# Kernel tuning notes

Hardware: AMD Instinct MI355X
Metric: run time of the kernel (lower is better)

## Reference

```python
import jax, jax.numpy as jnp
import numpy as np

EPS = 1e-8  # torch F.cosine_similarity eps


def setup_inputs() -> dict:
    key = jax.random.key(0)
    k1, k2, k3 = jax.random.split(key, 3)
    bn, cn, dim = 4096, 8192, 1024
    x = jax.random.normal(k1, (bn, dim), dtype=jnp.float32)
    positive = jax.random.normal(k2, (bn, dim), dtype=jnp.float32)
    negative = jax.random.normal(k3, (cn, dim), dtype=jnp.float32)
    return {"x": x, "positive": positive, "negative": negative}


def reference(x, positive, negative):
    bn = x.shape[0]
    nx = jnp.linalg.norm(x, axis=1)          # (bn,)
    npos = jnp.linalg.norm(positive, axis=1)  # (bn,)
    nneg = jnp.linalg.norm(negative, axis=1)  # (cn,)
    # positive cosine similarity, torch-style eps clamp on norm product
    sim = jnp.sum(x * positive, axis=1) / jnp.maximum(nx * npos, EPS)  # (bn,)
    # negative cosine similarities via one matmul instead of (bn,cn,dim) repeats
    neg_sim = (x @ negative.T) / jnp.maximum(nx[:, None] * nneg[None, :], EPS)  # (bn,cn)
    p = jnp.exp(sim) / jnp.sum(jnp.exp(neg_sim), axis=1)  # (bn,)
    loss = -jnp.sum(jnp.log(p)) / bn
    return loss
```

## Files before the change

### kernel.cpp

```cpp
#include <hip/hip_runtime.h>
#include <stdint.h>
#include <stddef.h>

#define DIM 1024
#define EPS 1e-8f

typedef __attribute__((ext_vector_type(4)))  int   i32x4;
typedef __attribute__((ext_vector_type(8)))  int   i32x8;
typedef __attribute__((ext_vector_type(4)))  float f32x4;

#define SCALE8 0x7B7B7B7B

__device__ __forceinline__ void async_copy16(const void* g, void* l) {
    __builtin_amdgcn_global_load_lds(
        (__attribute__((address_space(1))) void*)const_cast<void*>(g),
        (__attribute__((address_space(3))) void*)(l), 16, 0, 0);
}

__global__ __launch_bounds__(256)
void prep_all(const float* __restrict__ x, const float* __restrict__ pos,
              const float* __restrict__ neg,
              unsigned char* __restrict__ Xn, unsigned char* __restrict__ Nn,
              float* __restrict__ simOut, float* __restrict__ rowsum, int bn) {
    const int lane = threadIdx.x & 63;
    const int wave = threadIdx.x >> 6;
    const int grow = blockIdx.x * 4 + wave;
    const bool isX = grow < bn;
    const int row  = isX ? grow : grow - bn;
    const float* src = isX ? x : neg;
    unsigned char* dst = isX ? Xn : Nn;

    const float4* s = (const float4*)(src + (size_t)row * DIM);
    float4 xv[4], pv[4];
    float sxx = 0.f, spp = 0.f, sxp = 0.f;
#pragma unroll
    for (int i = 0; i < 4; i++) {
        xv[i] = s[lane + 64 * i];
        sxx += xv[i].x * xv[i].x + xv[i].y * xv[i].y + xv[i].z * xv[i].z + xv[i].w * xv[i].w;
    }
    if (isX) {
        const float4* p = (const float4*)(pos + (size_t)row * DIM);
#pragma unroll
        for (int i = 0; i < 4; i++) {
            pv[i] = p[lane + 64 * i];
            spp += pv[i].x * pv[i].x + pv[i].y * pv[i].y + pv[i].z * pv[i].z + pv[i].w * pv[i].w;
            sxp += xv[i].x * pv[i].x + xv[i].y * pv[i].y + xv[i].z * pv[i].z + xv[i].w * pv[i].w;
        }
#pragma unroll
        for (int off = 1; off < 64; off <<= 1) {
            sxx += __shfl_xor(sxx, off);
            spp += __shfl_xor(spp, off);
            sxp += __shfl_xor(sxp, off);
        }
    } else {
#pragma unroll
        for (int off = 1; off < 64; off <<= 1) sxx += __shfl_xor(sxx, off);
    }
    const float nx  = sqrtf(sxx);
    const float inv = (nx > 0.f) ? (16.f / nx) : 0.f;
    if (isX && lane == 0) {
        const float np = sqrtf(spp);
        simOut[row] = sxp / fmaxf(nx * np, EPS);
        rowsum[row] = 0.f;
    }
    unsigned int t;
    t = __builtin_amdgcn_cvt_pk_fp8_f32(xv[0].x * inv, xv[0].y * inv, 0, false);
    unsigned int q0 = __builtin_amdgcn_cvt_pk_fp8_f32(xv[0].z * inv, xv[0].w * inv, t, true);
    t = __builtin_amdgcn_cvt_pk_fp8_f32(xv[1].x * inv, xv[1].y * inv, 0, false);
    unsigned int q1 = __builtin_amdgcn_cvt_pk_fp8_f32(xv[1].z * inv, xv[1].w * inv, t, true);
    t = __builtin_amdgcn_cvt_pk_fp8_f32(xv[2].x * inv, xv[2].y * inv, 0, false);
    unsigned int q2 = __builtin_amdgcn_cvt_pk_fp8_f32(xv[2].z * inv, xv[2].w * inv, t, true);
    t = __builtin_amdgcn_cvt_pk_fp8_f32(xv[3].x * inv, xv[3].y * inv, 0, false);
    unsigned int q3 = __builtin_amdgcn_cvt_pk_fp8_f32(xv[3].z * inv, xv[3].w * inv, t, true);

    unsigned int* wr = (unsigned int*)(dst + (size_t)row * DIM);
    wr[lane]       = q0;
    wr[lane + 64]  = q1;
    wr[lane + 128] = q2;
    wr[lane + 192] = q3;
}

__global__ __launch_bounds__(256, 3)
void gemm_exp_rowsum(const unsigned char* __restrict__ Xn,
                     const unsigned char* __restrict__ Nn,
                     float* __restrict__ rowsum) {
    constexpr int KB = DIM;
    constexpr int BK = 128;
    __shared__ __align__(16) unsigned char Bsh[3][128 * BK];

    const int tid  = threadIdx.x;
    const int lane = tid & 63;
    const int wave = tid >> 6;

    const int nwg  = gridDim.x * gridDim.y;
    const int bid  = blockIdx.y * gridDim.x + blockIdx.x;
    const int swz  = (bid & 7) * (nwg >> 3) + (bid >> 3);
    const int rowBase = (swz / gridDim.x) * 128;
    const int colBase = (swz % gridDim.x) * 128;

    const int srow = lane >> 3;
    const int sch  = (lane & 7) ^ srow;
    const unsigned char* gB = Nn + (size_t)(colBase + wave * 32 + srow) * KB + sch * 16;

    const f32x4 fz = {0.f, 0.f, 0.f, 0.f};
    f32x4 acc[4][4];
#pragma unroll
    for (int mi = 0; mi < 4; mi++)
#pragma unroll
        for (int ni = 0; ni < 4; ni++) acc[mi][ni] = fz;

    const int m0   = (wave >> 1) * 64;
    const int n0   = (wave & 1) * 64;
    const int mrow = lane & 15;
    const int q    = lane >> 4;
    const int c0   = ((2 * q) ^ (mrow & 7)) << 4;

    const unsigned char* gAbase =
        Xn + (size_t)(rowBase + m0 + mrow) * KB + 32 * q;

    int boff[4];
#pragma unroll
    for (int i = 0; i < 4; i++) boff[i] = (n0 + 16 * i + mrow) * BK + c0;

#define STAGE(buf, stg)                                                        \
    do {                                                                       \
        const int kq = (stg) * BK;                                             \
        _Pragma("unroll")                                                      \
        for (int i = 0; i < 4; i++)                                            \
            async_copy16(gB + (size_t)(8 * i) * KB + kq,                       \
                         &Bsh[buf][(wave * 32 + 8 * i) * BK]);                 \
    } while (0)

    STAGE(0, 0);
    STAGE(1, 1);
    asm volatile("s_waitcnt vmcnt(4)\n\ts_barrier" ::: "memory");

#pragma unroll
    for (int w = 0; w < 8; w++) {
        const unsigned char* Bb = Bsh[w % 3];
        if (w <= 5) STAGE((w + 2) % 3, w + 2);
        const unsigned char* gAw = gAbase + w * BK;
        i32x8 Af[4], Bf[4];
#pragma unroll
        for (int mi = 0; mi < 4; mi++) {
            i32x4 lo = *(const i32x4*)(gAw + (size_t)(16 * mi) * KB);
            i32x4 hi = *(const i32x4*)(gAw + (size_t)(16 * mi) * KB + 16);
            Af[mi] = __builtin_shufflevector(lo, hi, 0, 1, 2, 3, 4, 5, 6, 7);
        }
#pragma unroll
        for (int i = 0; i < 4; i++) {
            i32x4 lo = *(const i32x4*)(Bb + boff[i]);
            i32x4 hi = *(const i32x4*)(Bb + (boff[i] ^ 16));
            Bf[i] = __builtin_shufflevector(lo, hi, 0, 1, 2, 3, 4, 5, 6, 7);
        }
        __builtin_amdgcn_s_setprio(1);
#pragma unroll
        for (int mi = 0; mi < 4; mi++)
#pragma unroll
            for (int ni = 0; ni < 4; ni++)
                acc[mi][ni] = __builtin_amdgcn_mfma_scale_f32_16x16x128_f8f6f4(
                    Af[mi], Bf[ni], acc[mi][ni], 0, 0, 0, SCALE8, 0, SCALE8);
        __builtin_amdgcn_s_setprio(0);
        if (w <= 5) {
            asm volatile("s_waitcnt vmcnt(4)\n\ts_barrier" ::: "memory");
        } else if (w == 6) {
            asm volatile("s_waitcnt vmcnt(0)\n\ts_barrier" ::: "memory");
        }
    }
#undef STAGE

#pragma unroll
    for (int mi = 0; mi < 4; mi++) {
        float rs0 = 0.f, rs1 = 0.f, rs2 = 0.f, rs3 = 0.f;
#pragma unroll
        for (int ni = 0; ni < 4; ni++) {
            rs0 += __expf(acc[mi][ni].x);
            rs1 += __expf(acc[mi][ni].y);
            rs2 += __expf(acc[mi][ni].z);
            rs3 += __expf(acc[mi][ni].w);
        }
#pragma unroll
        for (int off = 1; off < 16; off <<= 1) {
            rs0 += __shfl_xor(rs0, off);
            rs1 += __shfl_xor(rs1, off);
            rs2 += __shfl_xor(rs2, off);
            rs3 += __shfl_xor(rs3, off);
        }
        if ((lane & 15) == 0) {
            const int r = rowBase + m0 + mi * 16 + q * 4;
            atomicAdd(&rowsum[r + 0], rs0);
            atomicAdd(&rowsum[r + 1], rs1);
            atomicAdd(&rowsum[r + 2], rs2);
            atomicAdd(&rowsum[r + 3], rs3);
        }
    }
}

__global__ __launch_bounds__(1024)
void loss_kernel(const float* __restrict__ rowsum, const float* __restrict__ sim,
                 float* __restrict__ out, int bn) {
    const int tid  = threadIdx.x;
    const int lane = tid & 63;
    const int wave = tid >> 6;
    float acc = 0.f;
    for (int i = tid; i < bn; i += 1024) acc += logf(rowsum[i]) - sim[i];
#pragma unroll
    for (int off = 1; off < 64; off <<= 1) acc += __shfl_xor(acc, off);
    __shared__ float red[16];
    if (lane == 0) red[wave] = acc;
    __syncthreads();
    if (tid == 0) {
        float t = 0.f;
#pragma unroll
        for (int i = 0; i < 16; i++) t += red[i];
        out[0] = t / (float)bn;
    }
}

extern "C" void kernel_launch(void* const* d_in, const int* in_sizes, int n_in,
                              void* d_out, int out_size, void* d_ws, size_t ws_size,
                              hipStream_t stream) {
    const float* x   = (const float*)d_in[0];
    const float* pos = (const float*)d_in[1];
    const float* neg = (const float*)d_in[2];
    const int bn = in_sizes[0] / DIM;
    const int cn = in_sizes[2] / DIM;

    unsigned char* Xn = (unsigned char*)d_ws;
    unsigned char* Nn = Xn + (size_t)bn * DIM;
    float* sim    = (float*)(Nn + (size_t)cn * DIM);
    float* rowsum = sim + bn;

    prep_all<<<dim3((bn + cn) / 4), dim3(256), 0, stream>>>(x, pos, neg, Xn, Nn, sim, rowsum, bn);
    gemm_exp_rowsum<<<dim3(cn / 128, bn / 128), dim3(256), 0, stream>>>(Xn, Nn, rowsum);
    loss_kernel<<<dim3(1), dim3(1024), 0, stream>>>(rowsum, sim, (float*)d_out, bn);
}
```

Measured before the change: 188.2 us.

## Stage A tiles through LDS with double buffering instead of direct global loads

The A operand (normalized x in fp8) now goes into shared memory through async global-to-LDS copies alongside B, instead of being read directly from global memory into registers each k-step. The B pipeline drops from triple to double buffering and the occupancy hint falls from 3 to 2 blocks per CU. The intent is to hide A load latency and get swizzled, bank-friendly A fragment reads. In exchange the prefetch depth is shallower, each step waits for a full vmcnt(0), and LDS use rises, which may lower occupancy.

```diff
diff --git a/kernel.cpp b/kernel.cpp
--- a/kernel.cpp
+++ b/kernel.cpp
@@ -80,13 +80,14 @@
     wr[lane + 192] = q3;
 }
 
-__global__ __launch_bounds__(256, 3)
+__global__ __launch_bounds__(256, 2)
 void gemm_exp_rowsum(const unsigned char* __restrict__ Xn,
                      const unsigned char* __restrict__ Nn,
                      float* __restrict__ rowsum) {
     constexpr int KB = DIM;
     constexpr int BK = 128;
-    __shared__ __align__(16) unsigned char Bsh[3][128 * BK];
+    __shared__ __align__(16) unsigned char Ash[2][128 * BK];
+    __shared__ __align__(16) unsigned char Bsh[2][128 * BK];
 
     const int tid  = threadIdx.x;
     const int lane = tid & 63;
@@ -100,6 +101,7 @@
 
     const int srow = lane >> 3;
     const int sch  = (lane & 7) ^ srow;
+    const unsigned char* gA = Xn + (size_t)(rowBase + wave * 32 + srow) * KB + sch * 16;
     const unsigned char* gB = Nn + (size_t)(colBase + wave * 32 + srow) * KB + sch * 16;
 
     const f32x4 fz = {0.f, 0.f, 0.f, 0.f};
@@ -115,43 +117,41 @@
     const int q    = lane >> 4;
     const int c0   = ((2 * q) ^ (mrow & 7)) << 4;
 
-    const unsigned char* gAbase =
-        Xn + (size_t)(rowBase + m0 + mrow) * KB + 32 * q;
-
-    int boff[4];
-#pragma unroll
-    for (int i = 0; i < 4; i++) boff[i] = (n0 + 16 * i + mrow) * BK + c0;
+    int aoff[4], boff[4];
+#pragma unroll
+    for (int i = 0; i < 4; i++) {
+        aoff[i] = (m0 + 16 * i + mrow) * BK + c0;
+        boff[i] = (n0 + 16 * i + mrow) * BK + c0;
+    }
 
 #define STAGE(buf, stg)                                                        \
     do {                                                                       \
         const int kq = (stg) * BK;                                             \
         _Pragma("unroll")                                                      \
-        for (int i = 0; i < 4; i++)                                            \
+        for (int i = 0; i < 4; i++) {                                          \
+            async_copy16(gA + (size_t)(8 * i) * KB + kq,                       \
+                         &Ash[buf][(wave * 32 + 8 * i) * BK]);                 \
             async_copy16(gB + (size_t)(8 * i) * KB + kq,                       \
                          &Bsh[buf][(wave * 32 + 8 * i) * BK]);                 \
+        }                                                                      \
     } while (0)
 
     STAGE(0, 0);
-    STAGE(1, 1);
-    asm volatile("s_waitcnt vmcnt(4)\n\ts_barrier" ::: "memory");
+    asm volatile("s_waitcnt vmcnt(0)\n\ts_barrier" ::: "memory");
 
 #pragma unroll
     for (int w = 0; w < 8; w++) {
-        const unsigned char* Bb = Bsh[w % 3];
-        if (w <= 5) STAGE((w + 2) % 3, w + 2);
-        const unsigned char* gAw = gAbase + w * BK;
+        const int b = w & 1;
+        if (w < 7) STAGE(b ^ 1, w + 1);
         i32x8 Af[4], Bf[4];
 #pragma unroll
-        for (int mi = 0; mi < 4; mi++) {
-            i32x4 lo = *(const i32x4*)(gAw + (size_t)(16 * mi) * KB);
-            i32x4 hi = *(const i32x4*)(gAw + (size_t)(16 * mi) * KB + 16);
-            Af[mi] = __builtin_shufflevector(lo, hi, 0, 1, 2, 3, 4, 5, 6, 7);
-        }
-#pragma unroll
         for (int i = 0; i < 4; i++) {
-            i32x4 lo = *(const i32x4*)(Bb + boff[i]);
-            i32x4 hi = *(const i32x4*)(Bb + (boff[i] ^ 16));
-            Bf[i] = __builtin_shufflevector(lo, hi, 0, 1, 2, 3, 4, 5, 6, 7);
+            i32x4 alo = *(const i32x4*)(&Ash[b][aoff[i]]);
+            i32x4 ahi = *(const i32x4*)(&Ash[b][aoff[i] ^ 16]);
+            Af[i] = __builtin_shufflevector(alo, ahi, 0, 1, 2, 3, 4, 5, 6, 7);
+            i32x4 blo = *(const i32x4*)(&Bsh[b][boff[i]]);
+            i32x4 bhi = *(const i32x4*)(&Bsh[b][boff[i] ^ 16]);
+            Bf[i] = __builtin_shufflevector(blo, bhi, 0, 1, 2, 3, 4, 5, 6, 7);
         }
         __builtin_amdgcn_s_setprio(1);
 #pragma unroll
@@ -161,11 +161,8 @@
                 acc[mi][ni] = __builtin_amdgcn_mfma_scale_f32_16x16x128_f8f6f4(
                     Af[mi], Bf[ni], acc[mi][ni], 0, 0, 0, SCALE8, 0, SCALE8);
         __builtin_amdgcn_s_setprio(0);
-        if (w <= 5) {
-            asm volatile("s_waitcnt vmcnt(4)\n\ts_barrier" ::: "memory");
-        } else if (w == 6) {
+        if (w < 7)
             asm volatile("s_waitcnt vmcnt(0)\n\ts_barrier" ::: "memory");
-        }
     }
 #undef STAGE
 
```

New measurement: 184.3 us. 1.02x faster.
